# Kernel optimization log

Measured on AMD Instinct MI355X. Metric: run time of the kernel, lower is better.

The kernel has to match this reference:

```python
import jax, jax.numpy as jnp
import numpy as np

NUM_FEATURE = 128  # bins; linear in_features = NUM_FEATURE + 1
VECTOR_DIM = 64


def setup_inputs() -> dict:
    key = jax.random.key(0)
    k1, k2, k3 = jax.random.split(key, 3)
    x = jax.random.randint(k1, (8192, 200), 0, NUM_FEATURE + 1)
    # nn.Linear(num_feature+1, vector_dim): W is (out, in) = (64, 129)
    W = jax.random.normal(k2, (VECTOR_DIM, NUM_FEATURE + 1), dtype=jnp.float32) * 0.05
    b = jax.random.normal(k3, (VECTOR_DIM,), dtype=jnp.float32) * 0.05
    return {"x": x, "W": W, "b": b}


def reference(x, W, b):
    # embeddings = tril(ones)[x] has ones in columns 0..x (inclusive), so
    # embeddings @ W.T = sum_{j<=x} W[:, j] = cumsum(W, axis=1)[:, x].
    # This avoids materializing the (..., F+1) one-hot-prefix tensor.
    Wc = jnp.cumsum(W, axis=1)              # (D, F+1)
    out = jnp.take(Wc.T, x, axis=0) + b     # (8192, 200, D)
    return out
```

## Files before the change

### kernel.cpp

```cpp
#include <hip/hip_runtime.h>


constexpr int F1   = 129;
constexpr int D    = 64;
constexpr int ROWS = 8192 * 200;
constexpr int TBL_F = F1 * D;
constexpr int TBL4  = TBL_F / 4;

constexpr int BLOCKS = 1024;
constexpr int TPB    = 512;
constexpr int ROWS_PER_BLOCK = ROWS / BLOCKS;
constexpr int Q_PER_BLOCK    = ROWS_PER_BLOCK * D / 4;
constexpr int ITERS          = Q_PER_BLOCK / TPB;

typedef float floatx4 __attribute__((ext_vector_type(4)));

__global__ __launch_bounds__(TPB, 8) void embed_fused_kernel(
        const int*   __restrict__ x,
        const float* __restrict__ W,
        const float* __restrict__ b,
        float*       __restrict__ out) {
    __shared__ floatx4 lds_tbl[TBL4];
    __shared__ int     lds_x[ROWS_PER_BLOCK];
    float* tblf = (float*)lds_tbl;

    const int row0 = blockIdx.x * ROWS_PER_BLOCK;
    for (int i = threadIdx.x; i < ROWS_PER_BLOCK; i += TPB)
        lds_x[i] = x[row0 + i];

    if (threadIdx.x < D) {
        const int d = threadIdx.x;
        const float* wrow = W + d * F1;
        float acc = b[d];
        int j = 0;
#pragma unroll 1
        for (int c = 0; c < 16; ++c) {
            float v[8];
#pragma unroll
            for (int i = 0; i < 8; ++i) v[i] = wrow[j + i];
#pragma unroll
            for (int i = 0; i < 8; ++i) { acc += v[i]; tblf[(j + i) * D + d] = acc; }
            j += 8;
        }
        acc += wrow[128];
        tblf[128 * D + d] = acc;
    }
    __syncthreads();

    floatx4* out4 = (floatx4*)out + (size_t)blockIdx.x * Q_PER_BLOCK;
#pragma unroll 5
    for (int it = 0; it < ITERS; ++it) {
        int j    = it * TPB + threadIdx.x;
        int xi   = lds_x[j >> 4];
        floatx4 v = lds_tbl[xi * 16 + (j & 15)];
        out4[j] = v;
    }
}

extern "C" void kernel_launch(void* const* d_in, const int* in_sizes, int n_in,
                              void* d_out, int out_size, void* d_ws, size_t ws_size,
                              hipStream_t stream) {
    const int*   x = (const int*)  d_in[0];
    const float* W = (const float*)d_in[1];
    const float* b = (const float*)d_in[2];
    float* out = (float*)d_out;
    (void)d_ws; (void)ws_size;

    embed_fused_kernel<<<BLOCKS, TPB, 0, stream>>>(x, W, b, out);
}
```

Measured before the change: 420.3 us.

## Use fewer larger blocks with per-wave contiguous output and batched LDS gathers

Cuts the grid from 1024 blocks of 512 threads to 256 blocks of 256 threads, so each block rebuilds the cumsum table in LDS fewer times overall. Each wave now owns a contiguous slice of output rows. It issues 16 LDS gathers before its 16 global stores, which is meant to overlap LDS latency and keep stores in flight. The trade-off is far fewer resident waves per CU (256 blocks on roughly 256 CUs, one block each), so latency hiding depends on this batching. It also adds register pressure from the 16 float4 values.

```diff
diff --git a/kernel.cpp b/kernel.cpp
--- a/kernel.cpp
+++ b/kernel.cpp
@@ -7,15 +7,18 @@
 constexpr int TBL_F = F1 * D;
 constexpr int TBL4  = TBL_F / 4;
 
-constexpr int BLOCKS = 1024;
-constexpr int TPB    = 512;
+constexpr int BLOCKS = 256;
+constexpr int TPB    = 256;
 constexpr int ROWS_PER_BLOCK = ROWS / BLOCKS;
 constexpr int Q_PER_BLOCK    = ROWS_PER_BLOCK * D / 4;
-constexpr int ITERS          = Q_PER_BLOCK / TPB;
+constexpr int Q_PER_WAVE     = Q_PER_BLOCK / 4;
+constexpr int ROWS_PER_WAVE  = ROWS_PER_BLOCK / 4;
+constexpr int ITERS          = Q_PER_WAVE / 64;
+constexpr int BATCH          = 16;
 
 typedef float floatx4 __attribute__((ext_vector_type(4)));
 
-__global__ __launch_bounds__(TPB, 8) void embed_fused_kernel(
+__global__ __launch_bounds__(TPB) void embed_fused_kernel(
         const int*   __restrict__ x,
         const float* __restrict__ W,
         const float* __restrict__ b,
@@ -47,13 +50,25 @@
     }
     __syncthreads();
 
-    floatx4* out4 = (floatx4*)out + (size_t)blockIdx.x * Q_PER_BLOCK;
-#pragma unroll 5
-    for (int it = 0; it < ITERS; ++it) {
-        int j    = it * TPB + threadIdx.x;
-        int xi   = lds_x[j >> 4];
-        floatx4 v = lds_tbl[xi * 16 + (j & 15)];
-        out4[j] = v;
+    const int wave = threadIdx.x >> 6;
+    const int lane = threadIdx.x & 63;
+    const int quad = lane & 15;
+    const int xrow0 = wave * ROWS_PER_WAVE + (lane >> 4);
+    floatx4* wout = (floatx4*)out
+                  + (size_t)blockIdx.x * Q_PER_BLOCK
+                  + wave * Q_PER_WAVE + lane;
+
+#pragma unroll 1
+    for (int i = 0; i < ITERS; i += BATCH) {
+        floatx4 v[BATCH];
+#pragma unroll
+        for (int u = 0; u < BATCH; ++u) {
+            int xi = lds_x[xrow0 + (i + u) * 4];
+            v[u]   = lds_tbl[xi * 16 + quad];
+        }
+#pragma unroll
+        for (int u = 0; u < BATCH; ++u)
+            wout[(i + u) * 64] = v[u];
     }
 }
 
```

After: 424.0 us. Within noise of the previous version (+0.9%).
